# Optimization experiments

Hardware: AMD Instinct MI355X
Metric: run time of the kernel (lower is better)

The kernel has to match this reference:

```python
import jax, jax.numpy as jnp
import numpy as np

CONF_THRES = 0.25
MAX_DET = 300  # truncate to first 300 surviving rows per image


def setup_inputs() -> dict:
    key = jax.random.key(0)
    # [B, n_anchors, 5+nc]: (x, y, w, h, obj_conf, class scores...)
    prediction = jax.random.uniform(key, (16, 25200, 85), dtype=jnp.float32)
    return {"prediction": prediction}


def reference(prediction):
    # Original (multi_label path, no autolabel constants):
    #   per image: rows with obj_conf > conf_thres, in original order,
    #   truncated to first 300. We emit a fixed [B, 300, C] tensor with
    #   invalid slots zeroed (matches torch's zeros(0,6) empty semantics,
    #   padded to static shape for jit).
    mask = prediction[..., 4] > CONF_THRES                      # [B, N] bool
    # stable argsort of ~mask puts passing rows first, preserving order
    order = jnp.argsort(jnp.logical_not(mask), axis=1)[:, :MAX_DET]  # [B, 300]
    sel = jnp.take_along_axis(prediction, order[..., None], axis=1)  # [B, 300, C]
    valid = jnp.take_along_axis(mask, order, axis=1)                 # [B, 300]
    return sel * valid[..., None].astype(sel.dtype)
```

## Files before the change

kernel.cpp:

```cpp
#include <hip/hip_runtime.h>

#define BATCH 16
#define NANCH 25200
#define NCOLS 85
#define CONF_COL 4
#define CONF_THRES 0.25f
#define MAX_DET 300
#define BLOCK 1024
#define NWAVES (BLOCK / 64)

__global__ __launch_bounds__(BLOCK) void nms_prefilter_kernel(
    const float* __restrict__ pred, float* __restrict__ out) {
    __shared__ int sel_idx[MAX_DET];
    __shared__ int wave_sums[NWAVES];

    const int b = blockIdx.x;
    const int tid = threadIdx.x;
    const int lane = tid & 63;
    const int wave = tid >> 6;
    const float* img = pred + (size_t)b * NANCH * NCOLS;

    int base = 0;

    for (int chunk = 0; chunk < NANCH; chunk += BLOCK) {
        const int i = chunk + tid;
        int flag = 0;
        if (i < NANCH) {
            flag = (img[(size_t)i * NCOLS + CONF_COL] > CONF_THRES) ? 1 : 0;
        }
        unsigned long long ball = __ballot(flag);
        int excl_in_wave = __popcll(ball & ((1ull << lane) - 1ull));
        if (lane == 0) wave_sums[wave] = __popcll(ball);
        __syncthreads();
        int wave_offset = 0;
        for (int w = 0; w < wave; ++w) wave_offset += wave_sums[w];
        int chunk_total = wave_offset;
        for (int w = wave; w < NWAVES; ++w) chunk_total += wave_sums[w];

        int rank = base + wave_offset + excl_in_wave;
        if (flag && rank < MAX_DET) sel_idx[rank] = i;

        base += chunk_total;
        __syncthreads();
        if (base >= MAX_DET) break;
    }

    const int count = base < MAX_DET ? base : MAX_DET;
    float* dst = out + (size_t)b * MAX_DET * NCOLS;

    for (int t = tid; t < MAX_DET * NCOLS; t += BLOCK) {
        const int j = t / NCOLS;
        const int c = t - j * NCOLS;
        float v = 0.0f;
        if (j < count) {
            v = img[(size_t)sel_idx[j] * NCOLS + c];
        }
        dst[t] = v;
    }
}

extern "C" void kernel_launch(void* const* d_in, const int* in_sizes, int n_in,
                              void* d_out, int out_size, void* d_ws, size_t ws_size,
                              hipStream_t stream) {
    const float* pred = (const float*)d_in[0];
    float* out = (float*)d_out;
    nms_prefilter_kernel<<<BATCH, BLOCK, 0, stream>>>(pred, out);
}
```

Baseline: 174.9 us.

## Split scan and gather-copy into two kernels to parallelize the output copy

Separates the per-image compaction scan from the row gather. The scan kernel writes each image's count and selected row indices to workspace, and a new grid-wide copy kernel fills the output using many blocks instead of one block per image. This removes the bottleneck of only 16 blocks performing the whole copy. In exchange it adds a second kernel launch and a global-memory round trip for the indices.

Result: faster. 165.9 us (-5.2%).

```diff
diff --git a/kernel.cpp b/kernel.cpp
--- a/kernel.cpp
+++ b/kernel.cpp
@@ -8,9 +8,11 @@
 #define MAX_DET 300
 #define BLOCK 1024
 #define NWAVES (BLOCK / 64)
+#define WS_STRIDE (MAX_DET + 1)
+#define TOTAL_OUT (BATCH * MAX_DET * NCOLS)
 
-__global__ __launch_bounds__(BLOCK) void nms_prefilter_kernel(
-    const float* __restrict__ pred, float* __restrict__ out) {
+__global__ __launch_bounds__(BLOCK) void scan_kernel(
+    const float* __restrict__ pred, int* __restrict__ ws) {
     __shared__ int sel_idx[MAX_DET];
     __shared__ int wave_sums[NWAVES];
 
@@ -46,17 +48,30 @@
     }
 
     const int count = base < MAX_DET ? base : MAX_DET;
-    float* dst = out + (size_t)b * MAX_DET * NCOLS;
+    int* wsb = ws + b * WS_STRIDE;
+    if (tid == 0) wsb[0] = count;
+    for (int j = tid; j < MAX_DET; j += BLOCK) {
+        wsb[1 + j] = (j < count) ? sel_idx[j] : 0;
+    }
+}
 
-    for (int t = tid; t < MAX_DET * NCOLS; t += BLOCK) {
-        const int j = t / NCOLS;
-        const int c = t - j * NCOLS;
-        float v = 0.0f;
-        if (j < count) {
-            v = img[(size_t)sel_idx[j] * NCOLS + c];
-        }
-        dst[t] = v;
+__global__ __launch_bounds__(256) void copy_kernel(
+    const float* __restrict__ pred, const int* __restrict__ ws,
+    float* __restrict__ out) {
+    const int t = blockIdx.x * 256 + threadIdx.x;
+    if (t >= TOTAL_OUT) return;
+    const int b = t / (MAX_DET * NCOLS);
+    const int r = t - b * (MAX_DET * NCOLS);
+    const int j = r / NCOLS;
+    const int c = r - j * NCOLS;
+    const int* wsb = ws + b * WS_STRIDE;
+    const int count = wsb[0];
+    float v = 0.0f;
+    if (j < count) {
+        const int row = wsb[1 + j];
+        v = pred[((size_t)b * NANCH + row) * NCOLS + c];
     }
+    out[t] = v;
 }
 
 extern "C" void kernel_launch(void* const* d_in, const int* in_sizes, int n_in,
@@ -64,5 +79,7 @@
                               hipStream_t stream) {
     const float* pred = (const float*)d_in[0];
     float* out = (float*)d_out;
-    nms_prefilter_kernel<<<BATCH, BLOCK, 0, stream>>>(pred, out);
+    int* ws = (int*)d_ws;
+    scan_kernel<<<BATCH, BLOCK, 0, stream>>>(pred, ws);
+    copy_kernel<<<(TOTAL_OUT + 255) / 256, 256, 0, stream>>>(pred, ws, out);
 }
```
